# Optimization experiments

Measured on AMD Instinct MI355X. Metric: run time of the kernel, lower is better.

Reference implementation:

```python
import jax, jax.numpy as jnp
import numpy as np
import math

N_BITS = 8
NUM_GROUPS = 32
NUM_HEADS = 8
EPS = 1e-5


def fake_quant(x):
    # UniformAffineQuantizer: dynamic per-tensor asymmetric 8-bit fake quant
    levels = 2 ** N_BITS - 1
    xmin = jnp.minimum(x.min(), 0.0)
    xmax = jnp.maximum(x.max(), 0.0)
    scale = jnp.maximum((xmax - xmin) / levels, 1e-8)
    zp = jnp.round(-xmin / scale)
    xq = jnp.clip(jnp.round(x / scale) + zp, 0, levels)
    return (xq - zp) * scale


def group_norm(x, w, b):
    # x: (B, C, T)
    B, C, T = x.shape
    xg = x.reshape(B, NUM_GROUPS, C // NUM_GROUPS, T)
    mean = xg.mean(axis=(2, 3), keepdims=True)
    var = xg.var(axis=(2, 3), keepdims=True)
    xg = (xg - mean) * jax.lax.rsqrt(var + EPS)
    return xg.reshape(B, C, T) * w[None, :, None] + b[None, :, None]


def setup_inputs() -> dict:
    key = jax.random.key(0)
    ks = jax.random.split(key, 7)
    C = 512
    x = jax.random.normal(ks[0], (8, C, 32, 32), dtype=jnp.float32)
    gn_w = jnp.ones((C,), jnp.float32)
    gn_b = jnp.zeros((C,), jnp.float32)
    qkv_w = jax.random.normal(ks[1], (3 * C, C), jnp.float32) * (1.0 / math.sqrt(C))
    qkv_b = jax.random.normal(ks[2], (3 * C,), jnp.float32) * 0.01
    proj_w = jax.random.normal(ks[3], (C, C), jnp.float32) * (1.0 / math.sqrt(C))
    proj_b = jax.random.normal(ks[4], (C,), jnp.float32) * 0.01
    return {"x": x, "gn_w": gn_w, "gn_b": gn_b, "qkv_w": qkv_w,
            "qkv_b": qkv_b, "proj_w": proj_w, "proj_b": proj_b}


def reference(x, gn_w, gn_b, qkv_w, qkv_b, proj_w, proj_b):
    b, c, *spatial = x.shape
    T = int(np.prod(spatial))
    xf = x.reshape(b, c, T)                       # (B, C, T)
    h = group_norm(xf, gn_w, gn_b)
    qkv = jnp.einsum('oc,bct->bot', qkv_w, h) + qkv_b[None, :, None]  # (B, 3C, T)
    qkv = qkv.reshape(b * NUM_HEADS, -1, T)       # (B*H, 3*ch, T)
    ch = qkv.shape[1] // 3
    q, k, v = jnp.split(qkv, 3, axis=1)
    q = fake_quant(q)
    k = fake_quant(k)
    v = fake_quant(v)
    scale = 1.0 / math.sqrt(math.sqrt(ch))
    w = jnp.einsum('bct,bcs->bts', q * scale, k * scale)
    w = jax.nn.softmax(w.astype(jnp.float32), axis=-1).astype(q.dtype)
    a = jnp.einsum('bts,bcs->bct', w, v)          # (B*H, ch, T)
    a = a.reshape(b, c, T)
    a = jnp.einsum('oc,bct->bot', proj_w, a) + proj_b[None, :, None]
    return (xf + a).reshape(b, c, *spatial)
```

## Files before the change

kernel.cpp:

```cpp
#include <hip/hip_runtime.h>

typedef __attribute__((ext_vector_type(8))) __bf16 bf16x8;
typedef __attribute__((ext_vector_type(4))) __bf16 bf16x4;
typedef __attribute__((ext_vector_type(4))) float  f32x4;


static constexpr size_t QKV_OFF = 0;
static constexpr size_t HT_OFF  = 50331648;
static constexpr size_t WQ_OFF  = HT_OFF + 8388608;
static constexpr size_t WP_OFF  = WQ_OFF + 1572864;
static constexpr size_t MM_OFF  = WP_OFF + 524288;
static constexpr size_t KI_OFF  = MM_OFF + 4096;
static constexpr size_t VI_OFF  = KI_OFF + 8388608;
static constexpr size_t QI_OFF  = VI_OFF + 8388608;
static constexpr size_t NEED_NEW = QI_OFF + 8388608;

__device__ __forceinline__ unsigned encf(float f) {
    unsigned u = __float_as_uint(f);
    return (u & 0x80000000u) ? ~u : (u | 0x80000000u);
}
__device__ __forceinline__ float decf(unsigned e) {
    unsigned u = (e & 0x80000000u) ? (e & 0x7fffffffu) : ~e;
    return __uint_as_float(u);
}
__device__ __forceinline__ float dqi(float x, float inv_s, float zp) {
    float y = rintf(x * inv_s);
    return fminf(fmaxf(y, -zp), 255.0f - zp);
}
__device__ __forceinline__ f32x4 mfma16(bf16x8 a, bf16x8 b, f32x4 c) {
    return __builtin_amdgcn_mfma_f32_16x16x32_bf16(a, b, c, 0, 0, 0);
}
__device__ __forceinline__ float exp2i(float x) {
    float r;
    asm("v_exp_f32 %0, %1" : "=v"(r) : "v"(x));
    return r;
}
__device__ __forceinline__ void glds16(const __bf16* g, __bf16* l) {
    __builtin_amdgcn_global_load_lds((const __attribute__((address_space(1))) void*)g,
                                     (__attribute__((address_space(3))) void*)l, 16, 0, 0);
}
template <int N> __device__ __forceinline__ void waitv() {
    asm volatile("s_waitcnt vmcnt(%0)" :: "n"(N) : "memory");
}
__device__ __forceinline__ void bar_raw() {
    asm volatile("s_barrier" ::: "memory");
}

__global__ __launch_bounds__(256) void gnprep(const float* __restrict__ x,
                                              const float* __restrict__ w,
                                              const float* __restrict__ bv,
                                              __bf16* __restrict__ hT,
                                              const float* __restrict__ qw,
                                              __bf16* __restrict__ wq,
                                              const float* __restrict__ pw,
                                              __bf16* __restrict__ wp,
                                              unsigned* __restrict__ mm) {
    int bid = blockIdx.x, tid = threadIdx.x;
    if (bid < 1024) {
        if (bid == 0 && tid < 3) { mm[2 * tid] = 0xFFFFFFFFu; mm[2 * tid + 1] = 0u; }
        if (bid < 768) {
            int i = bid * 256 + tid;
            float4 v = ((const float4*)qw)[i];
            bf16x4 o = {(__bf16)v.x, (__bf16)v.y, (__bf16)v.z, (__bf16)v.w};
            ((bf16x4*)wq)[i] = o;
        } else {
            int i = (bid - 768) * 256 + tid;
            float4 v = ((const float4*)pw)[i];
            bf16x4 o = {(__bf16)v.x, (__bf16)v.y, (__bf16)v.z, (__bf16)v.w};
            ((bf16x4*)wp)[i] = o;
        }
        return;
    }
    int blk = bid - 1024;
    int b = blk >> 5, g = blk & 31;
    const float* xp = x + (size_t)(b * 512 + g * 16) * 1024;

    float4 v[16];
    float sum = 0.f, ss = 0.f;
#pragma unroll
    for (int i = 0; i < 16; ++i) {
        v[i] = *(const float4*)(xp + (size_t)i * 1024 + tid * 4);
        sum += v[i].x + v[i].y + v[i].z + v[i].w;
        ss  += v[i].x * v[i].x + v[i].y * v[i].y + v[i].z * v[i].z + v[i].w * v[i].w;
    }
#pragma unroll
    for (int m = 1; m < 64; m <<= 1) {
        sum += __shfl_xor(sum, m);
        ss  += __shfl_xor(ss, m);
    }
    __shared__ float s1[4], s2[4];
    int wid = tid >> 6;
    if ((tid & 63) == 0) { s1[wid] = sum; s2[wid] = ss; }
    __syncthreads();
    sum = s1[0] + s1[1] + s1[2] + s1[3];
    ss  = s2[0] + s2[1] + s2[2] + s2[3];
    float mean = sum * (1.0f / 16384.0f);
    float var  = ss * (1.0f / 16384.0f) - mean * mean;
    float rstd = rsqrtf(var + 1e-5f);

    float wc[16], bc[16];
#pragma unroll
    for (int c = 0; c < 16; ++c) { wc[c] = w[g * 16 + c] * rstd; bc[c] = bv[g * 16 + c]; }

#pragma unroll
    for (int j = 0; j < 4; ++j) {
        int t = tid * 4 + j;
        bf16x8 o0, o1;
#pragma unroll
        for (int c = 0; c < 8; ++c)
            o0[c] = (__bf16)(((&v[c].x)[j] - mean) * wc[c] + bc[c]);
#pragma unroll
        for (int c = 0; c < 8; ++c)
            o1[c] = (__bf16)(((&v[c + 8].x)[j] - mean) * wc[c + 8] + bc[c + 8]);
        __bf16* hp = hT + ((size_t)b * 1024 + t) * 512 + g * 16;
        *(bf16x8*)hp = o0;
        *(bf16x8*)(hp + 8) = o1;
    }
}

template <int MTILE, int MOT, bool MINMAX, bool RESID>
__global__ __launch_bounds__(256, 4) void mgemm4(const __bf16* __restrict__ A,
                                                 const __bf16* __restrict__ Bt,
                                                 const float* __restrict__ bias,
                                                 const float* __restrict__ resid,
                                                 float* __restrict__ out,
                                                 int M, unsigned* __restrict__ mm) {
    constexpr int NF  = (MTILE == 128) ? 4 : 2;
    constexpr int ASZ = MTILE * 32;
    constexpr int BSZ = 128 * 32;
    constexpr int LA  = MTILE / 64;
    constexpr int L   = LA + 2;
    constexpr int STG = 2 * (ASZ + BSZ) * 2;
    constexpr int CSB = 64 * 132 * 4;
    __shared__ __attribute__((aligned(16))) char smem_raw[(STG > CSB) ? STG : CSB];
    __bf16* sA0 = (__bf16*)smem_raw;
    __bf16* sA1 = sA0 + ASZ;
    __bf16* sB0 = sA1 + ASZ;
    __bf16* sB1 = sB0 + BSZ;
    __shared__ float smn[4], smx[4];

    int tid = threadIdx.x;
    int l = tid & 63, w = tid >> 6;
    int lo = l & 15, hi = l >> 4;

    int f = blockIdx.x;
    constexpr int NWG = MOT * 64;
    int wg = (f & 7) * (NWG / 8) + (f >> 3);
    int mo = wg % MOT, nb = wg / MOT;
    int nt = nb & 7, b = nb >> 3;

    const __bf16* Ap = A + (size_t)mo * MTILE * 512;
    const __bf16* Bp = Bt + ((size_t)b * 1024 + (size_t)nt * 128) * 512;
    int m0 = (MTILE == 128) ? (w >> 1) * 64 : 0;
    int n0 = (MTILE == 128) ? (w & 1) * 64 : w * 32;
    f32x4 acc[4][NF] = {};

    auto STAGE = [&](__bf16* dA, __bf16* dB, int k0) {
#pragma unroll
        for (int p = 0; p < LA; ++p) {
            int lin = p * 2048 + tid * 8;
            int row = lin >> 5;
            int sc = ((tid & 3) ^ (row & 3)) << 3;
            glds16(Ap + (size_t)row * 512 + k0 + sc, dA + lin);
        }
#pragma unroll
        for (int p = 0; p < 2; ++p) {
            int lin = p * 2048 + tid * 8;
            int row = lin >> 5;
            int sc = ((tid & 3) ^ (row & 3)) << 3;
            glds16(Bp + (size_t)row * 512 + k0 + sc, dB + lin);
        }
    };
    auto COMPUTE = [&](const __bf16* cA, const __bf16* cB) {
        int rcoff = (hi ^ (lo & 3)) << 3;
        bf16x8 af[4], bfr[NF];
#pragma unroll
        for (int i = 0; i < 4; ++i) af[i] = *(const bf16x8*)&cA[(m0 + 16 * i + lo) * 32 + rcoff];
#pragma unroll
        for (int j = 0; j < NF; ++j) bfr[j] = *(const bf16x8*)&cB[(n0 + 16 * j + lo) * 32 + rcoff];
#pragma unroll
        for (int i = 0; i < 4; ++i)
#pragma unroll
            for (int j = 0; j < NF; ++j) acc[i][j] = mfma16(af[i], bfr[j], acc[i][j]);
    };

    STAGE(sA0, sB0, 0);
#pragma unroll
    for (int kp = 0; kp < 16; kp += 2) {
        if (kp + 1 < 16) { STAGE(sA1, sB1, (kp + 1) * 32); waitv<L>(); } else { waitv<0>(); }
        bar_raw();
        COMPUTE(sA0, sB0);
        bar_raw();
        if (kp + 2 < 16) { STAGE(sA0, sB0, (kp + 2) * 32); waitv<L>(); } else { waitv<0>(); }
        bar_raw();
        COMPUTE(sA1, sB1);
        bar_raw();
    }

    float* cs = (float*)smem_raw;
    float mn = 1e30f, mx = -1e30f;
    constexpr int NH = (MTILE == 128) ? 2 : 1;
#pragma unroll
    for (int h = 0; h < NH; ++h) {
        __syncthreads();
        if (MTILE == 64 || (w >> 1) == h) {
#pragma unroll
            for (int i = 0; i < 4; ++i)
#pragma unroll
                for (int r = 0; r < 4; ++r) {
                    int rl = 16 * i + hi * 4 + r;
                    float bi = bias[mo * MTILE + h * 64 + rl];
#pragma unroll
                    for (int j = 0; j < NF; ++j)
                        cs[rl * 132 + n0 + 16 * j + lo] = acc[i][j][r] + bi;
                }
        }
        __syncthreads();
#pragma unroll
        for (int it = 0; it < 8; ++it) {
            int lin = it * 256 + tid;
            int rr = lin >> 5, cc = (lin & 31) << 2;
            float4 v = *(const float4*)&cs[rr * 132 + cc];
            if (MINMAX) {
                mn = fminf(mn, fminf(fminf(v.x, v.y), fminf(v.z, v.w)));
                mx = fmaxf(mx, fmaxf(fmaxf(v.x, v.y), fmaxf(v.z, v.w)));
            }
            int grow = mo * MTILE + h * 64 + rr;
            size_t gaddr = ((size_t)b * M + grow) * 1024 + nt * 128 + cc;
            if (RESID) {
                float4 rv = *(const float4*)&resid[gaddr];
                v.x += rv.x; v.y += rv.y; v.z += rv.z; v.w += rv.w;
            }
            *(float4*)&out[gaddr] = v;
        }
    }

    if (MINMAX) {
#pragma unroll
        for (int msk = 1; msk < 64; msk <<= 1) {
            mn = fminf(mn, __shfl_xor(mn, msk));
            mx = fmaxf(mx, __shfl_xor(mx, msk));
        }
        if (l == 0) { smn[w] = mn; smx[w] = mx; }
        __syncthreads();
        if (tid == 0) {
            mn = fminf(fminf(smn[0], smn[1]), fminf(smn[2], smn[3]));
            mx = fmaxf(fmaxf(smx[0], smx[1]), fmaxf(smx[2], smx[3]));
            int id = mo >> 2;
            atomicMin(&mm[2 * id], encf(mn));
            atomicMax(&mm[2 * id + 1], encf(mx));
        }
    }
}

__global__ __launch_bounds__(256) void quant_qkv(const float* __restrict__ qkv,
                                                 const unsigned* __restrict__ mm,
                                                 __bf16* __restrict__ qi,
                                                 __bf16* __restrict__ ki,
                                                 __bf16* __restrict__ vi) {
    int bh = blockIdx.x, tt = blockIdx.y;
    int b = bh >> 3, hh = bh & 7;
    int t0 = tt * 64;
    const float* qg = qkv + (size_t)(b * 1536 + hh * 192) * 1024;
    const float* kg = qg + 65536;
    const float* vg = qg + 131072;

    float mn0 = fminf(decf(mm[0]), 0.f), mx0 = fmaxf(decf(mm[1]), 0.f);
    float qsc = fmaxf((mx0 - mn0) * (1.f / 255.f), 1e-8f), qzp = rintf(-mn0 / qsc);
    float mn1 = fminf(decf(mm[2]), 0.f), mx1 = fmaxf(decf(mm[3]), 0.f);
    float ksc = fmaxf((mx1 - mn1) * (1.f / 255.f), 1e-8f), kzp = rintf(-mn1 / ksc);
    float mn2 = fminf(decf(mm[4]), 0.f), mx2 = fmaxf(decf(mm[5]), 0.f);
    float vsc = fmaxf((mx2 - mn2) * (1.f / 255.f), 1e-8f), vzp = rintf(-mn2 / vsc);
    float inv_q = 1.f / qsc, inv_k = 1.f / ksc, inv_v = 1.f / vsc;

    __shared__ __bf16 sT[64][68];
    int tid = threadIdx.x;
    int cr = tid >> 4, t4 = tid & 15;
    int s = tid >> 2, c0 = (tid & 3) * 16;

    __bf16* vd = vi + (size_t)bh * 65536;
#pragma unroll
    for (int r = 0; r < 4; ++r) {
        int c = 16 * r + cr;
        float4 v = *(const float4*)(vg + (size_t)c * 1024 + t0 + t4 * 4);
        bf16x4 o = {(__bf16)dqi(v.x, inv_v, vzp), (__bf16)dqi(v.y, inv_v, vzp),
                    (__bf16)dqi(v.z, inv_v, vzp), (__bf16)dqi(v.w, inv_v, vzp)};
        *(bf16x4*)(vd + (size_t)c * 1024 + t0 + t4 * 4) = o;
    }

#pragma unroll
    for (int r = 0; r < 4; ++r) {
        int c = 16 * r + cr;
        float4 v = *(const float4*)(kg + (size_t)c * 1024 + t0 + t4 * 4);
        sT[t4 * 4 + 0][c] = (__bf16)dqi(v.x, inv_k, kzp);
        sT[t4 * 4 + 1][c] = (__bf16)dqi(v.y, inv_k, kzp);
        sT[t4 * 4 + 2][c] = (__bf16)dqi(v.z, inv_k, kzp);
        sT[t4 * 4 + 3][c] = (__bf16)dqi(v.w, inv_k, kzp);
    }
    __syncthreads();
    {
        bf16x8 a0 = *(const bf16x8*)&sT[s][c0];
        bf16x8 a1 = *(const bf16x8*)&sT[s][c0 + 8];
        __bf16* kd = ki + ((size_t)bh * 1024 + t0 + s) * 64 + c0;
        *(bf16x8*)kd = a0;
        *(bf16x8*)(kd + 8) = a1;
    }
    __syncthreads();

#pragma unroll
    for (int r = 0; r < 4; ++r) {
        int c = 16 * r + cr;
        float4 v = *(const float4*)(qg + (size_t)c * 1024 + t0 + t4 * 4);
        sT[t4 * 4 + 0][c] = (__bf16)dqi(v.x, inv_q, qzp);
        sT[t4 * 4 + 1][c] = (__bf16)dqi(v.y, inv_q, qzp);
        sT[t4 * 4 + 2][c] = (__bf16)dqi(v.z, inv_q, qzp);
        sT[t4 * 4 + 3][c] = (__bf16)dqi(v.w, inv_q, qzp);
    }
    __syncthreads();
    {
        bf16x8 a0 = *(const bf16x8*)&sT[s][c0];
        bf16x8 a1 = *(const bf16x8*)&sT[s][c0 + 8];
        __bf16* qd = qi + ((size_t)bh * 1024 + t0 + s) * 64 + c0;
        *(bf16x8*)qd = a0;
        *(bf16x8*)(qd + 8) = a1;
    }
}

__global__ __launch_bounds__(256) void attn4(const __bf16* __restrict__ qi,
                                             const __bf16* __restrict__ ki,
                                             const __bf16* __restrict__ vi,
                                             const unsigned* __restrict__ mm,
                                             __bf16* __restrict__ aT) {
    int f = blockIdx.x;
    int bh = (f & 7) * 8 + ((f >> 3) & 7);
    int tt = f >> 6;
    int b = bh >> 3, hh = bh & 7;
    int t0 = tt * 64;
    const __bf16* kb = ki + (size_t)bh * 65536;
    const __bf16* vb = vi + (size_t)bh * 65536;

    float mn0 = fminf(decf(mm[0]), 0.f), mx0 = fmaxf(decf(mm[1]), 0.f);
    float qsc = fmaxf((mx0 - mn0) * (1.f / 255.f), 1e-8f);
    float mn1 = fminf(decf(mm[2]), 0.f), mx1 = fmaxf(decf(mm[3]), 0.f);
    float ksc = fmaxf((mx1 - mn1) * (1.f / 255.f), 1e-8f);
    float mn2 = fminf(decf(mm[4]), 0.f), mx2 = fmaxf(decf(mm[5]), 0.f);
    float vsc = fmaxf((mx2 - mn2) * (1.f / 255.f), 1e-8f);
    float alpha2 = qsc * ksc * 0.125f * 1.4426950408889634f;
    float thr = 11.5415603f / alpha2;

    __shared__ __bf16 sh[64][72];
    __shared__ __bf16 kS[64 * 64];
    __shared__ __bf16 vS[64 * 64];
    int tid = threadIdx.x;
    int l = tid & 63, w = tid >> 6;
    int lo = l & 15, hi = l >> 4;

    const __bf16* qrow = qi + ((size_t)bh * 1024 + t0 + 16 * w + lo) * 64;
    bf16x8 qf0 = *(const bf16x8*)(qrow + hi * 8);
    bf16x8 qf1 = *(const bf16x8*)(qrow + 32 + hi * 8);

    int srow = tid >> 2, sc2 = (tid & 3) * 2;
    int swz0 = (sc2 ^ (srow & 7)) << 3;
    int swz1 = ((sc2 + 1) ^ (srow & 7)) << 3;
    const __bf16* kROW = kb + (size_t)srow * 64;
    const __bf16* vROW = vb + (size_t)srow * 1024;
    int lx = lo & 7;
    int rc0 = (hi ^ lx) << 3;
    int rc1 = ((4 + hi) ^ lx) << 3;

    bf16x8 kr0 = *(const bf16x8*)(kROW + sc2 * 8);
    bf16x8 kr1 = *(const bf16x8*)(kROW + sc2 * 8 + 8);
    bf16x8 vr0 = *(const bf16x8*)(vROW + sc2 * 8);
    bf16x8 vr1 = *(const bf16x8*)(vROW + sc2 * 8 + 8);

    f32x4 acc0 = {}, acc1 = {}, acc2 = {}, acc3 = {};
    float m_run = -1e30f, l_run = 0.f;

    for (int st = 0; st < 16; ++st) {
        __syncthreads();
        *(bf16x8*)(kS + srow * 64 + swz0) = kr0;
        *(bf16x8*)(kS + srow * 64 + swz1) = kr1;
        *(bf16x8*)(vS + srow * 64 + swz0) = vr0;
        *(bf16x8*)(vS + srow * 64 + swz1) = vr1;
        __syncthreads();
        if (st < 15) {
            kr0 = *(const bf16x8*)(kROW + (st + 1) * 4096 + sc2 * 8);
            kr1 = *(const bf16x8*)(kROW + (st + 1) * 4096 + sc2 * 8 + 8);
            vr0 = *(const bf16x8*)(vROW + (st + 1) * 64 + sc2 * 8);
            vr1 = *(const bf16x8*)(vROW + (st + 1) * 64 + sc2 * 8 + 8);
        }

        f32x4 sf[4] = {};
        __builtin_amdgcn_s_setprio(1);
#pragma unroll
        for (int sm = 0; sm < 4; ++sm)
            sf[sm] = mfma16(*(const bf16x8*)(kS + (16 * sm + lo) * 64 + rc0), qf0, sf[sm]);
#pragma unroll
        for (int sm = 0; sm < 4; ++sm)
            sf[sm] = mfma16(*(const bf16x8*)(kS + (16 * sm + lo) * 64 + rc1), qf1, sf[sm]);
        __builtin_amdgcn_s_setprio(0);

        float tm = -1e30f;
#pragma unroll
        for (int sm = 0; sm < 4; ++sm) {
            float a = fmaxf(sf[sm][0], sf[sm][1]);
            float c = fmaxf(sf[sm][2], sf[sm][3]);
            tm = fmaxf(tm, fmaxf(a, c));
        }
        tm = fmaxf(tm, __shfl_xor(tm, 16));
        tm = fmaxf(tm, __shfl_xor(tm, 32));
        if (!__all(tm <= m_run + thr)) {
            float mnew = fmaxf(m_run, tm);
            float fr = exp2i(alpha2 * (m_run - mnew));
            acc0 *= fr; acc1 *= fr; acc2 *= fr; acc3 *= fr;
            l_run *= fr;
            m_run = mnew;
        }
        float cc = -alpha2 * m_run;
        float ts = 0.f;
#pragma unroll
        for (int sm = 0; sm < 4; ++sm)
#pragma unroll
            for (int r = 0; r < 4; ++r) {
                float p = exp2i(fmaf(sf[sm][r], alpha2, cc));
                sf[sm][r] = p;
                ts += p;
            }
        ts += __shfl_xor(ts, 16);
        ts += __shfl_xor(ts, 32);
        l_run += ts;

#pragma unroll
        for (int sm = 0; sm < 4; ++sm) {
            bf16x4 pb = {(__bf16)sf[sm][0], (__bf16)sf[sm][1], (__bf16)sf[sm][2], (__bf16)sf[sm][3]};
            *(bf16x4*)&sh[16 * w + lo][16 * sm + hi * 4] = pb;
        }
        bf16x8 pf0 = *(const bf16x8*)&sh[16 * w + lo][hi * 8];
        bf16x8 pf1 = *(const bf16x8*)&sh[16 * w + lo][32 + hi * 8];

        __builtin_amdgcn_s_setprio(1);
        acc0 = mfma16(*(const bf16x8*)(vS + (lo) * 64 + rc0), pf0, acc0);
        acc1 = mfma16(*(const bf16x8*)(vS + (16 + lo) * 64 + rc0), pf0, acc1);
        acc2 = mfma16(*(const bf16x8*)(vS + (32 + lo) * 64 + rc0), pf0, acc2);
        acc3 = mfma16(*(const bf16x8*)(vS + (48 + lo) * 64 + rc0), pf0, acc3);
        acc0 = mfma16(*(const bf16x8*)(vS + (lo) * 64 + rc1), pf1, acc0);
        acc1 = mfma16(*(const bf16x8*)(vS + (16 + lo) * 64 + rc1), pf1, acc1);
        acc2 = mfma16(*(const bf16x8*)(vS + (32 + lo) * 64 + rc1), pf1, acc2);
        acc3 = mfma16(*(const bf16x8*)(vS + (48 + lo) * 64 + rc1), pf1, acc3);
        __builtin_amdgcn_s_setprio(0);
    }

    float rl = vsc / l_run;
    __syncthreads();
    {
        bf16x4 o0 = {(__bf16)(acc0[0] * rl), (__bf16)(acc0[1] * rl), (__bf16)(acc0[2] * rl), (__bf16)(acc0[3] * rl)};
        bf16x4 o1 = {(__bf16)(acc1[0] * rl), (__bf16)(acc1[1] * rl), (__bf16)(acc1[2] * rl), (__bf16)(acc1[3] * rl)};
        bf16x4 o2 = {(__bf16)(acc2[0] * rl), (__bf16)(acc2[1] * rl), (__bf16)(acc2[2] * rl), (__bf16)(acc2[3] * rl)};
        bf16x4 o3 = {(__bf16)(acc3[0] * rl), (__bf16)(acc3[1] * rl), (__bf16)(acc3[2] * rl), (__bf16)(acc3[3] * rl)};
        *(bf16x4*)&sh[16 * w + lo][0  + hi * 4] = o0;
        *(bf16x4*)&sh[16 * w + lo][16 + hi * 4] = o1;
        *(bf16x4*)&sh[16 * w + lo][32 + hi * 4] = o2;
        *(bf16x4*)&sh[16 * w + lo][48 + hi * 4] = o3;
    }
    __syncthreads();
    __bf16* ap = aT + ((size_t)b * 1024 + t0 + (tid >> 2)) * 512 + hh * 64;
    bf16x8 v0 = *(const bf16x8*)&sh[tid >> 2][(tid & 3) * 8];
    bf16x8 v1 = *(const bf16x8*)&sh[tid >> 2][32 + (tid & 3) * 8];
    *(bf16x8*)(ap + (tid & 3) * 8) = v0;
    *(bf16x8*)(ap + 32 + (tid & 3) * 8) = v1;
}

__global__ __launch_bounds__(256) void attn_mfma(const float* __restrict__ qkv,
                                                 const unsigned* __restrict__ mm,
                                                 __bf16* __restrict__ aT) {
    int f = blockIdx.x;
    int bh = (f & 7) * 8 + ((f >> 3) & 7);
    int tt = f >> 6;
    int b = bh >> 3, hh = bh & 7;
    int t0 = tt * 64;
    const float* qg = qkv + (size_t)(b * 1536 + hh * 192) * 1024;
    const float* kg = qg + (size_t)64 * 1024;
    const float* vg = qg + (size_t)128 * 1024;

    float mn0 = fminf(decf(mm[0]), 0.f), mx0 = fmaxf(decf(mm[1]), 0.f);
    float qsc = fmaxf((mx0 - mn0) * (1.f / 255.f), 1e-8f), qzp = rintf(-mn0 / qsc);
    float mn1 = fminf(decf(mm[2]), 0.f), mx1 = fmaxf(decf(mm[3]), 0.f);
    float ksc = fmaxf((mx1 - mn1) * (1.f / 255.f), 1e-8f), kzp = rintf(-mn1 / ksc);
    float mn2 = fminf(decf(mm[4]), 0.f), mx2 = fmaxf(decf(mm[5]), 0.f);
    float vsc = fmaxf((mx2 - mn2) * (1.f / 255.f), 1e-8f), vzp = rintf(-mn2 / vsc);
    float inv_q = 1.f / qsc, inv_k = 1.f / ksc, inv_v = 1.f / vsc;
    float alpha = qsc * ksc * 0.125f;

    __shared__ __bf16 qT[64][72];
    __shared__ __bf16 kT[64][72];
    __shared__ __bf16 vL[64][72];
    __shared__ __bf16 pL[4][16][72];

    int tid = threadIdx.x;
    int l = tid & 63, w = tid >> 6;
    int lo = l & 15, hi = l >> 4;
    int c0 = (tid >> 4) * 4;
    int tl = tid & 15;

#pragma unroll
    for (int r = 0; r < 4; ++r) {
        int t = tl + 16 * r;
        float y0 = dqi(qg[(size_t)(c0 + 0) * 1024 + t0 + t], inv_q, qzp);
        float y1 = dqi(qg[(size_t)(c0 + 1) * 1024 + t0 + t], inv_q, qzp);
        float y2 = dqi(qg[(size_t)(c0 + 2) * 1024 + t0 + t], inv_q, qzp);
        float y3 = dqi(qg[(size_t)(c0 + 3) * 1024 + t0 + t], inv_q, qzp);
        bf16x4 o = {(__bf16)y0, (__bf16)y1, (__bf16)y2, (__bf16)y3};
        *(bf16x4*)&qT[t][c0] = o;
    }
    __syncthreads();
    bf16x8 qf0 = *(const bf16x8*)&qT[16 * w + lo][hi * 8];
    bf16x8 qf1 = *(const bf16x8*)&qT[16 * w + lo][32 + hi * 8];

    f32x4 acc0 = {}, acc1 = {}, acc2 = {}, acc3 = {};
    float m_run = -1e30f, l_run = 0.f;

    for (int st = 0; st < 16; ++st) {
        int s0 = st * 64;
        __syncthreads();
#pragma unroll
        for (int r = 0; r < 4; ++r) {
            int srow = tl + 16 * r;
            float y0 = dqi(kg[(size_t)(c0 + 0) * 1024 + s0 + srow], inv_k, kzp);
            float y1 = dqi(kg[(size_t)(c0 + 1) * 1024 + s0 + srow], inv_k, kzp);
            float y2 = dqi(kg[(size_t)(c0 + 2) * 1024 + s0 + srow], inv_k, kzp);
            float y3 = dqi(kg[(size_t)(c0 + 3) * 1024 + s0 + srow], inv_k, kzp);
            bf16x4 ok = {(__bf16)y0, (__bf16)y1, (__bf16)y2, (__bf16)y3};
            *(bf16x4*)&kT[srow][c0] = ok;
            int c = (tid >> 4) + 16 * r;
            float4 vv = *(const float4*)(vg + (size_t)c * 1024 + s0 + (tid & 15) * 4);
            bf16x4 ov = {(__bf16)dqi(vv.x, inv_v, vzp), (__bf16)dqi(vv.y, inv_v, vzp),
                         (__bf16)dqi(vv.z, inv_v, vzp), (__bf16)dqi(vv.w, inv_v, vzp)};
            *(bf16x4*)&vL[c][(tid & 15) * 4] = ov;
        }
        __syncthreads();

        f32x4 sf[4] = {};
#pragma unroll
        for (int sm = 0; sm < 4; ++sm)
            sf[sm] = mfma16(*(const bf16x8*)&kT[16 * sm + lo][hi * 8], qf0, sf[sm]);
#pragma unroll
        for (int sm = 0; sm < 4; ++sm)
            sf[sm] = mfma16(*(const bf16x8*)&kT[16 * sm + lo][32 + hi * 8], qf1, sf[sm]);

        float tm = -1e30f;
#pragma unroll
        for (int sm = 0; sm < 4; ++sm)
#pragma unroll
            for (int r = 0; r < 4; ++r) { sf[sm][r] *= alpha; tm = fmaxf(tm, sf[sm][r]); }
        tm = fmaxf(tm, __shfl_xor(tm, 16));
        tm = fmaxf(tm, __shfl_xor(tm, 32));
        float mnew = fmaxf(m_run, tm);
        float ts = 0.f;
#pragma unroll
        for (int sm = 0; sm < 4; ++sm)
#pragma unroll
            for (int r = 0; r < 4; ++r) {
                float p = __expf(sf[sm][r] - mnew);
                sf[sm][r] = p;
                ts += p;
            }
        ts += __shfl_xor(ts, 16);
        ts += __shfl_xor(ts, 32);
        float fr = __expf(m_run - mnew);
        l_run = l_run * fr + ts;
        m_run = mnew;
        acc0 *= fr; acc1 *= fr; acc2 *= fr; acc3 *= fr;

#pragma unroll
        for (int sm = 0; sm < 4; ++sm) {
            bf16x4 pb = {(__bf16)sf[sm][0], (__bf16)sf[sm][1], (__bf16)sf[sm][2], (__bf16)sf[sm][3]};
            *(bf16x4*)&pL[w][lo][16 * sm + hi * 4] = pb;
        }
        bf16x8 pf0 = *(const bf16x8*)&pL[w][lo][hi * 8];
        bf16x8 pf1 = *(const bf16x8*)&pL[w][lo][32 + hi * 8];
        acc0 = mfma16(*(const bf16x8*)&vL[lo][hi * 8], pf0, acc0);
        acc1 = mfma16(*(const bf16x8*)&vL[16 + lo][hi * 8], pf0, acc1);
        acc2 = mfma16(*(const bf16x8*)&vL[32 + lo][hi * 8], pf0, acc2);
        acc3 = mfma16(*(const bf16x8*)&vL[48 + lo][hi * 8], pf0, acc3);
        acc0 = mfma16(*(const bf16x8*)&vL[lo][32 + hi * 8], pf1, acc0);
        acc1 = mfma16(*(const bf16x8*)&vL[16 + lo][32 + hi * 8], pf1, acc1);
        acc2 = mfma16(*(const bf16x8*)&vL[32 + lo][32 + hi * 8], pf1, acc2);
        acc3 = mfma16(*(const bf16x8*)&vL[48 + lo][32 + hi * 8], pf1, acc3);
    }

    float rl = vsc / l_run;
    __syncthreads();
    {
        bf16x4 o0 = {(__bf16)(acc0[0] * rl), (__bf16)(acc0[1] * rl), (__bf16)(acc0[2] * rl), (__bf16)(acc0[3] * rl)};
        bf16x4 o1 = {(__bf16)(acc1[0] * rl), (__bf16)(acc1[1] * rl), (__bf16)(acc1[2] * rl), (__bf16)(acc1[3] * rl)};
        bf16x4 o2 = {(__bf16)(acc2[0] * rl), (__bf16)(acc2[1] * rl), (__bf16)(acc2[2] * rl), (__bf16)(acc2[3] * rl)};
        bf16x4 o3 = {(__bf16)(acc3[0] * rl), (__bf16)(acc3[1] * rl), (__bf16)(acc3[2] * rl), (__bf16)(acc3[3] * rl)};
        *(bf16x4*)&qT[16 * w + lo][0  + hi * 4] = o0;
        *(bf16x4*)&qT[16 * w + lo][16 + hi * 4] = o1;
        *(bf16x4*)&qT[16 * w + lo][32 + hi * 4] = o2;
        *(bf16x4*)&qT[16 * w + lo][48 + hi * 4] = o3;
    }
    __syncthreads();
    __bf16* ap = aT + ((size_t)b * 1024 + t0 + (tid >> 2)) * 512 + hh * 64;
    bf16x8 v0 = *(const bf16x8*)&qT[tid >> 2][(tid & 3) * 8];
    bf16x8 v1 = *(const bf16x8*)&qT[tid >> 2][32 + (tid & 3) * 8];
    *(bf16x8*)(ap + (tid & 3) * 8) = v0;
    *(bf16x8*)(ap + 32 + (tid & 3) * 8) = v1;
}

extern "C" void kernel_launch(void* const* d_in, const int* in_sizes, int n_in,
                              void* d_out, int out_size, void* d_ws, size_t ws_size,
                              hipStream_t stream) {
    const float* x      = (const float*)d_in[0];
    const float* gn_w   = (const float*)d_in[1];
    const float* gn_b   = (const float*)d_in[2];
    const float* qkv_w  = (const float*)d_in[3];
    const float* qkv_b  = (const float*)d_in[4];
    const float* proj_w = (const float*)d_in[5];
    const float* proj_b = (const float*)d_in[6];
    char* ws = (char*)d_ws;
    float*    qkv = (float*)(ws + QKV_OFF);
    __bf16*   hT  = (__bf16*)(ws + HT_OFF);
    __bf16*   wq  = (__bf16*)(ws + WQ_OFF);
    __bf16*   wp  = (__bf16*)(ws + WP_OFF);
    unsigned* mm  = (unsigned*)(ws + MM_OFF);
    __bf16*   ki  = (__bf16*)(ws + KI_OFF);
    __bf16*   vi  = (__bf16*)(ws + VI_OFF);
    __bf16*   qi  = (__bf16*)(ws + QI_OFF);
    float* out = (float*)d_out;

    gnprep<<<1280, 256, 0, stream>>>(x, gn_w, gn_b, hT, qkv_w, wq, proj_w, wp, mm);
    mgemm4<128, 12, true, false><<<768, 256, 0, stream>>>(wq, hT, qkv_b, nullptr, qkv, 1536, mm);
    if (ws_size >= NEED_NEW) {
        quant_qkv<<<dim3(64, 16), 256, 0, stream>>>(qkv, mm, qi, ki, vi);
        attn4<<<1024, 256, 0, stream>>>(qi, ki, vi, mm, hT);
    } else {
        attn_mfma<<<1024, 256, 0, stream>>>(qkv, mm, hT);
    }
    mgemm4<64, 8, false, true><<<512, 256, 0, stream>>>(wp, hT, proj_b, x, out, 512, nullptr);
}
```

Baseline: 106.2 us.

## Replace global min/max atomics with per-block partials and double GEMM K-tile

The QKV GEMM epilogue now writes a per-workgroup min/max partial for each of q, k and v into a workspace array instead of doing encoded atomicMin/atomicMax on global counters. The quant and attention kernels each reduce the 256 partials per tensor with wave shuffles, which also removes the init write from gnprep. Separately, the GEMM K-step grows from 32 to 64 with an 8-way XOR swizzle, which halves the number of barriers per tile but doubles shared memory and lowers the occupancy hint from 4 to 2. Every attention block now repeats the partial reduction, adding redundant loads and barriers at kernel start.

```diff
diff --git a/kernel.cpp b/kernel.cpp
--- a/kernel.cpp
+++ b/kernel.cpp
@@ -10,19 +10,11 @@
 static constexpr size_t WQ_OFF  = HT_OFF + 8388608;
 static constexpr size_t WP_OFF  = WQ_OFF + 1572864;
 static constexpr size_t MM_OFF  = WP_OFF + 524288;
-static constexpr size_t KI_OFF  = MM_OFF + 4096;
+static constexpr size_t KI_OFF  = MM_OFF + 8192;
 static constexpr size_t VI_OFF  = KI_OFF + 8388608;
 static constexpr size_t QI_OFF  = VI_OFF + 8388608;
 static constexpr size_t NEED_NEW = QI_OFF + 8388608;
 
-__device__ __forceinline__ unsigned encf(float f) {
-    unsigned u = __float_as_uint(f);
-    return (u & 0x80000000u) ? ~u : (u | 0x80000000u);
-}
-__device__ __forceinline__ float decf(unsigned e) {
-    unsigned u = (e & 0x80000000u) ? (e & 0x7fffffffu) : ~e;
-    return __uint_as_float(u);
-}
 __device__ __forceinline__ float dqi(float x, float inv_s, float zp) {
     float y = rintf(x * inv_s);
     return fminf(fmaxf(y, -zp), 255.0f - zp);
@@ -44,6 +36,24 @@
 }
 __device__ __forceinline__ void bar_raw() {
     asm volatile("s_barrier" ::: "memory");
+}
+
+__device__ __forceinline__ void red_mm(const float* __restrict__ pmm, int id, int tid,
+                                       float* sred, float& mn_out, float& mx_out) {
+    float mn = pmm[id * 512 + tid * 2];
+    float mx = pmm[id * 512 + tid * 2 + 1];
+#pragma unroll
+    for (int m = 1; m < 64; m <<= 1) {
+        mn = fminf(mn, __shfl_xor(mn, m));
+        mx = fmaxf(mx, __shfl_xor(mx, m));
+    }
+    if ((tid & 63) == 0) { sred[(tid >> 6) * 2] = mn; sred[(tid >> 6) * 2 + 1] = mx; }
+    __syncthreads();
+    mn = fminf(fminf(sred[0], sred[2]), fminf(sred[4], sred[6]));
+    mx = fmaxf(fmaxf(sred[1], sred[3]), fmaxf(sred[5], sred[7]));
+    __syncthreads();
+    mn_out = fminf(mn, 0.0f);
+    mx_out = fmaxf(mx, 0.0f);
 }
 
 __global__ __launch_bounds__(256) void gnprep(const float* __restrict__ x,
@@ -53,11 +63,9 @@
                                               const float* __restrict__ qw,
                                               __bf16* __restrict__ wq,
                                               const float* __restrict__ pw,
-                                              __bf16* __restrict__ wp,
-                                              unsigned* __restrict__ mm) {
+                                              __bf16* __restrict__ wp) {
     int bid = blockIdx.x, tid = threadIdx.x;
     if (bid < 1024) {
-        if (bid == 0 && tid < 3) { mm[2 * tid] = 0xFFFFFFFFu; mm[2 * tid + 1] = 0u; }
         if (bid < 768) {
             int i = bid * 256 + tid;
             float4 v = ((const float4*)qw)[i];
@@ -119,17 +127,17 @@
 }
 
 template <int MTILE, int MOT, bool MINMAX, bool RESID>
-__global__ __launch_bounds__(256, 4) void mgemm4(const __bf16* __restrict__ A,
+__global__ __launch_bounds__(256, 2) void mgemm5(const __bf16* __restrict__ A,
                                                  const __bf16* __restrict__ Bt,
                                                  const float* __restrict__ bias,
                                                  const float* __restrict__ resid,
                                                  float* __restrict__ out,
-                                                 int M, unsigned* __restrict__ mm) {
+                                                 int M, float* __restrict__ pmm) {
     constexpr int NF  = (MTILE == 128) ? 4 : 2;
-    constexpr int ASZ = MTILE * 32;
-    constexpr int BSZ = 128 * 32;
-    constexpr int LA  = MTILE / 64;
-    constexpr int L   = LA + 2;
+    constexpr int ASZ = MTILE * 64;
+    constexpr int BSZ = 128 * 64;
+    constexpr int LA  = MTILE / 32;
+    constexpr int L   = LA + 4;
     constexpr int STG = 2 * (ASZ + BSZ) * 2;
     constexpr int CSB = 64 * 132 * 4;
     __shared__ __attribute__((aligned(16))) char smem_raw[(STG > CSB) ? STG : CSB];
@@ -154,44 +162,46 @@
     int m0 = (MTILE == 128) ? (w >> 1) * 64 : 0;
     int n0 = (MTILE == 128) ? (w & 1) * 64 : w * 32;
     f32x4 acc[4][NF] = {};
+    int scd = tid & 7;
 
     auto STAGE = [&](__bf16* dA, __bf16* dB, int k0) {
 #pragma unroll
         for (int p = 0; p < LA; ++p) {
             int lin = p * 2048 + tid * 8;
-            int row = lin >> 5;
-            int sc = ((tid & 3) ^ (row & 3)) << 3;
-            glds16(Ap + (size_t)row * 512 + k0 + sc, dA + lin);
-        }
-#pragma unroll
-        for (int p = 0; p < 2; ++p) {
+            int row = lin >> 6;
+            glds16(Ap + (size_t)row * 512 + k0 + ((scd ^ (row & 7)) << 3), dA + lin);
+        }
+#pragma unroll
+        for (int p = 0; p < 4; ++p) {
             int lin = p * 2048 + tid * 8;
-            int row = lin >> 5;
-            int sc = ((tid & 3) ^ (row & 3)) << 3;
-            glds16(Bp + (size_t)row * 512 + k0 + sc, dB + lin);
+            int row = lin >> 6;
+            glds16(Bp + (size_t)row * 512 + k0 + ((scd ^ (row & 7)) << 3), dB + lin);
         }
     };
     auto COMPUTE = [&](const __bf16* cA, const __bf16* cB) {
-        int rcoff = (hi ^ (lo & 3)) << 3;
-        bf16x8 af[4], bfr[NF];
-#pragma unroll
-        for (int i = 0; i < 4; ++i) af[i] = *(const bf16x8*)&cA[(m0 + 16 * i + lo) * 32 + rcoff];
-#pragma unroll
-        for (int j = 0; j < NF; ++j) bfr[j] = *(const bf16x8*)&cB[(n0 + 16 * j + lo) * 32 + rcoff];
-#pragma unroll
-        for (int i = 0; i < 4; ++i)
-#pragma unroll
-            for (int j = 0; j < NF; ++j) acc[i][j] = mfma16(af[i], bfr[j], acc[i][j]);
+#pragma unroll
+        for (int kk = 0; kk < 2; ++kk) {
+            int rch = ((kk * 4 + hi) ^ (lo & 7)) << 3;
+            bf16x8 af[4], bfr[NF];
+#pragma unroll
+            for (int i = 0; i < 4; ++i) af[i] = *(const bf16x8*)&cA[(m0 + 16 * i + lo) * 64 + rch];
+#pragma unroll
+            for (int j = 0; j < NF; ++j) bfr[j] = *(const bf16x8*)&cB[(n0 + 16 * j + lo) * 64 + rch];
+#pragma unroll
+            for (int i = 0; i < 4; ++i)
+#pragma unroll
+                for (int j = 0; j < NF; ++j) acc[i][j] = mfma16(af[i], bfr[j], acc[i][j]);
+        }
     };
 
     STAGE(sA0, sB0, 0);
 #pragma unroll
-    for (int kp = 0; kp < 16; kp += 2) {
-        if (kp + 1 < 16) { STAGE(sA1, sB1, (kp + 1) * 32); waitv<L>(); } else { waitv<0>(); }
+    for (int kp = 0; kp < 8; kp += 2) {
+        if (kp + 1 < 8) { STAGE(sA1, sB1, (kp + 1) * 64); waitv<L>(); } else { waitv<0>(); }
         bar_raw();
         COMPUTE(sA0, sB0);
         bar_raw();
-        if (kp + 2 < 16) { STAGE(sA0, sB0, (kp + 2) * 32); waitv<L>(); } else { waitv<0>(); }
+        if (kp + 2 < 8) { STAGE(sA0, sB0, (kp + 2) * 64); waitv<L>(); } else { waitv<0>(); }
         bar_raw();
         COMPUTE(sA1, sB1);
         bar_raw();
@@ -247,14 +257,15 @@
             mn = fminf(fminf(smn[0], smn[1]), fminf(smn[2], smn[3]));
             mx = fmaxf(fmaxf(smx[0], smx[1]), fmaxf(smx[2], smx[3]));
             int id = mo >> 2;
-            atomicMin(&mm[2 * id], encf(mn));
-            atomicMax(&mm[2 * id + 1], encf(mx));
+            int slot = nb * 4 + (mo & 3);
+            pmm[id * 512 + slot * 2]     = mn;
+            pmm[id * 512 + slot * 2 + 1] = mx;
         }
     }
 }
 
 __global__ __launch_bounds__(256) void quant_qkv(const float* __restrict__ qkv,
-                                                 const unsigned* __restrict__ mm,
+                                                 const float* __restrict__ pmm,
                                                  __bf16* __restrict__ qi,
                                                  __bf16* __restrict__ ki,
                                                  __bf16* __restrict__ vi) {
@@ -264,17 +275,19 @@
     const float* qg = qkv + (size_t)(b * 1536 + hh * 192) * 1024;
     const float* kg = qg + 65536;
     const float* vg = qg + 131072;
-
-    float mn0 = fminf(decf(mm[0]), 0.f), mx0 = fmaxf(decf(mm[1]), 0.f);
+    int tid = threadIdx.x;
+
+    __shared__ float sred[8];
+    float mn0, mx0, mn1, mx1, mn2, mx2;
+    red_mm(pmm, 0, tid, sred, mn0, mx0);
+    red_mm(pmm, 1, tid, sred, mn1, mx1);
+    red_mm(pmm, 2, tid, sred, mn2, mx2);
     float qsc = fmaxf((mx0 - mn0) * (1.f / 255.f), 1e-8f), qzp = rintf(-mn0 / qsc);
-    float mn1 = fminf(decf(mm[2]), 0.f), mx1 = fmaxf(decf(mm[3]), 0.f);
     float ksc = fmaxf((mx1 - mn1) * (1.f / 255.f), 1e-8f), kzp = rintf(-mn1 / ksc);
-    float mn2 = fminf(decf(mm[4]), 0.f), mx2 = fmaxf(decf(mm[5]), 0.f);
     float vsc = fmaxf((mx2 - mn2) * (1.f / 255.f), 1e-8f), vzp = rintf(-mn2 / vsc);
     float inv_q = 1.f / qsc, inv_k = 1.f / ksc, inv_v = 1.f / vsc;
 
     __shared__ __bf16 sT[64][68];
-    int tid = threadIdx.x;
     int cr = tid >> 4, t4 = tid & 15;
     int s = tid >> 2, c0 = (tid & 3) * 16;
 
@@ -329,7 +342,7 @@
 __global__ __launch_bounds__(256) void attn4(const __bf16* __restrict__ qi,
                                              const __bf16* __restrict__ ki,
                                              const __bf16* __restrict__ vi,
-                                             const unsigned* __restrict__ mm,
+                                             const float* __restrict__ pmm,
                                              __bf16* __restrict__ aT) {
     int f = blockIdx.x;
     int bh = (f & 7) * 8 + ((f >> 3) & 7);
@@ -338,12 +351,15 @@
     int t0 = tt * 64;
     const __bf16* kb = ki + (size_t)bh * 65536;
     const __bf16* vb = vi + (size_t)bh * 65536;
-
-    float mn0 = fminf(decf(mm[0]), 0.f), mx0 = fmaxf(decf(mm[1]), 0.f);
+    int tid = threadIdx.x;
+
+    __shared__ float sred[8];
+    float mn0, mx0, mn1, mx1, mn2, mx2;
+    red_mm(pmm, 0, tid, sred, mn0, mx0);
+    red_mm(pmm, 1, tid, sred, mn1, mx1);
+    red_mm(pmm, 2, tid, sred, mn2, mx2);
     float qsc = fmaxf((mx0 - mn0) * (1.f / 255.f), 1e-8f);
-    float mn1 = fminf(decf(mm[2]), 0.f), mx1 = fmaxf(decf(mm[3]), 0.f);
     float ksc = fmaxf((mx1 - mn1) * (1.f / 255.f), 1e-8f);
-    float mn2 = fminf(decf(mm[4]), 0.f), mx2 = fmaxf(decf(mm[5]), 0.f);
     float vsc = fmaxf((mx2 - mn2) * (1.f / 255.f), 1e-8f);
     float alpha2 = qsc * ksc * 0.125f * 1.4426950408889634f;
     float thr = 11.5415603f / alpha2;
@@ -351,7 +367,6 @@
     __shared__ __bf16 sh[64][72];
     __shared__ __bf16 kS[64 * 64];
     __shared__ __bf16 vS[64 * 64];
-    int tid = threadIdx.x;
     int l = tid & 63, w = tid >> 6;
     int lo = l & 15, hi = l >> 4;
 
@@ -471,7 +486,7 @@
 }
 
 __global__ __launch_bounds__(256) void attn_mfma(const float* __restrict__ qkv,
-                                                 const unsigned* __restrict__ mm,
+                                                 const float* __restrict__ pmm,
                                                  __bf16* __restrict__ aT) {
     int f = blockIdx.x;
     int bh = (f & 7) * 8 + ((f >> 3) & 7);
@@ -481,12 +496,15 @@
     const float* qg = qkv + (size_t)(b * 1536 + hh * 192) * 1024;
     const float* kg = qg + (size_t)64 * 1024;
     const float* vg = qg + (size_t)128 * 1024;
-
-    float mn0 = fminf(decf(mm[0]), 0.f), mx0 = fmaxf(decf(mm[1]), 0.f);
+    int tid = threadIdx.x;
+
+    __shared__ float sred[8];
+    float mn0, mx0, mn1, mx1, mn2, mx2;
+    red_mm(pmm, 0, tid, sred, mn0, mx0);
+    red_mm(pmm, 1, tid, sred, mn1, mx1);
+    red_mm(pmm, 2, tid, sred, mn2, mx2);
     float qsc = fmaxf((mx0 - mn0) * (1.f / 255.f), 1e-8f), qzp = rintf(-mn0 / qsc);
-    float mn1 = fminf(decf(mm[2]), 0.f), mx1 = fmaxf(decf(mm[3]), 0.f);
     float ksc = fmaxf((mx1 - mn1) * (1.f / 255.f), 1e-8f), kzp = rintf(-mn1 / ksc);
-    float mn2 = fminf(decf(mm[4]), 0.f), mx2 = fmaxf(decf(mm[5]), 0.f);
     float vsc = fmaxf((mx2 - mn2) * (1.f / 255.f), 1e-8f), vzp = rintf(-mn2 / vsc);
     float inv_q = 1.f / qsc, inv_k = 1.f / ksc, inv_v = 1.f / vsc;
     float alpha = qsc * ksc * 0.125f;
@@ -496,7 +514,6 @@
     __shared__ __bf16 vL[64][72];
     __shared__ __bf16 pL[4][16][72];
 
-    int tid = threadIdx.x;
     int l = tid & 63, w = tid >> 6;
     int lo = l & 15, hi = l >> 4;
     int c0 = (tid >> 4) * 4;
@@ -623,19 +640,19 @@
     __bf16*   hT  = (__bf16*)(ws + HT_OFF);
     __bf16*   wq  = (__bf16*)(ws + WQ_OFF);
     __bf16*   wp  = (__bf16*)(ws + WP_OFF);
-    unsigned* mm  = (unsigned*)(ws + MM_OFF);
+    float*    pmm = (float*)(ws + MM_OFF);
     __bf16*   ki  = (__bf16*)(ws + KI_OFF);
     __bf16*   vi  = (__bf16*)(ws + VI_OFF);
     __bf16*   qi  = (__bf16*)(ws + QI_OFF);
     float* out = (float*)d_out;
 
-    gnprep<<<1280, 256, 0, stream>>>(x, gn_w, gn_b, hT, qkv_w, wq, proj_w, wp, mm);
-    mgemm4<128, 12, true, false><<<768, 256, 0, stream>>>(wq, hT, qkv_b, nullptr, qkv, 1536, mm);
+    gnprep<<<1280, 256, 0, stream>>>(x, gn_w, gn_b, hT, qkv_w, wq, proj_w, wp);
+    mgemm5<128, 12, true, false><<<768, 256, 0, stream>>>(wq, hT, qkv_b, nullptr, qkv, 1536, pmm);
     if (ws_size >= NEED_NEW) {
-        quant_qkv<<<dim3(64, 16), 256, 0, stream>>>(qkv, mm, qi, ki, vi);
-        attn4<<<1024, 256, 0, stream>>>(qi, ki, vi, mm, hT);
+        quant_qkv<<<dim3(64, 16), 256, 0, stream>>>(qkv, pmm, qi, ki, vi);
+        attn4<<<1024, 256, 0, stream>>>(qi, ki, vi, pmm, hT);
     } else {
-        attn_mfma<<<1024, 256, 0, stream>>>(qkv, mm, hT);
-    }
-    mgemm4<64, 8, false, true><<<512, 256, 0, stream>>>(wp, hT, proj_b, x, out, 512, nullptr);
-}
+        attn_mfma<<<1024, 256, 0, stream>>>(qkv, pmm, hT);
+    }
+    mgemm5<64, 8, false, true><<<512, 256, 0, stream>>>(wp, hT, proj_b, x, out, 512, nullptr);
+}
```

Result: no change. 104.8 us (-1.3%).
